# Kernel optimization log

Hardware: AMD Instinct MI355X
Metric: run time of the kernel (lower is better)

Reference implementation:

```python
import jax, jax.numpy as jnp
import numpy as np

B, T, D, H = 4, 2048, 1024, 16
HD = D // H  # head_dim = 64


def setup_inputs() -> dict:
    key = jax.random.key(0)
    ks = jax.random.split(key, 7)
    x = jax.random.normal(ks[0], (B, T, D), dtype=jnp.float32)
    engagement = jax.random.uniform(ks[1], (B, T), dtype=jnp.float32)
    mask = jax.random.uniform(ks[2], (B, T)) < 0.1  # True = masked-out key
    s = 1.0 / np.sqrt(D)
    qkv_w = jax.random.normal(ks[3], (3 * D, D), dtype=jnp.float32) * s
    qkv_b = jax.random.normal(ks[4], (3 * D,), dtype=jnp.float32) * 0.02
    out_w = jax.random.normal(ks[5], (D, D), dtype=jnp.float32) * s
    out_b = jax.random.normal(ks[6], (D,), dtype=jnp.float32) * 0.02
    return {"x": x, "engagement": engagement, "mask": mask,
            "qkv_w": qkv_w, "qkv_b": qkv_b, "out_w": out_w, "out_b": out_b}


def reference(x, engagement, mask, qkv_w, qkv_b, out_w, out_b):
    b, t, d = x.shape
    qkv = x @ qkv_w.T + qkv_b                       # [B,T,3D]
    q, k, v = jnp.split(qkv, 3, axis=-1)
    # [B,T,D] -> [B,H,T,HD]
    to_heads = lambda a: a.reshape(b, t, H, HD).transpose(0, 2, 1, 3)
    q, k, v = to_heads(q), to_heads(k), to_heads(v)
    attn = jnp.einsum('bhqd,bhkd->bhqk', q, k) / jnp.sqrt(jnp.float32(HD))
    log_g = jnp.log(jnp.clip(engagement, 1e-6))     # [B,T] per-key bias
    attn = attn + log_g[:, None, None, :]
    attn = jnp.where(mask[:, None, None, :], jnp.float32(-1e9), attn)
    p = jax.nn.softmax(attn, axis=-1)
    o = jnp.einsum('bhqk,bhkd->bhqd', p, v)         # [B,H,T,HD]
    o = o.transpose(0, 2, 1, 3).reshape(b, t, d)    # [B,T,D]
    return o @ out_w.T + out_b
```

## Files before the change

### kernel.cpp

```cpp
#include <hip/hip_runtime.h>
#include <math.h>

#define B_  4
#define T_  2048
#define D_  1024
#define H_  16
#define HD_ 64

typedef unsigned short ushort_t;
typedef unsigned int uint_t;
typedef __attribute__((ext_vector_type(8))) short bf16x8;
typedef __attribute__((ext_vector_type(4))) float f32x4;

#define SC_LOG2 0.1803368801111243f

__device__ inline ushort_t f2bf(float f) {
  uint_t u = __float_as_uint(f);
  u += 0x7fffu + ((u >> 16) & 1u);
  return (ushort_t)(u >> 16);
}
__device__ inline ushort_t f2bf_fast(float f) {
  return (ushort_t)((__float_as_uint(f) + 0x8000u) >> 16);
}
__device__ inline uint_t cvtpk_bf16(float lo, float hi) {
  uint_t r;
  asm("v_cvt_pk_bf16_f32 %0, %1, %2" : "=v"(r) : "v"(lo), "v"(hi));
  return r;
}

__device__ inline void gload_lds16(const ushort_t* g, ushort_t* l) {
  __builtin_amdgcn_global_load_lds(
      (const __attribute__((address_space(1))) unsigned int*)g,
      (__attribute__((address_space(3))) unsigned int*)l, 16, 0, 0);
}

__global__ __launch_bounds__(256) void cvt_bf16(const float* __restrict__ in,
                                                ushort_t* __restrict__ out, int n) {
  int i = (blockIdx.x * 256 + threadIdx.x) * 4;
  if (i + 3 < n) {
    float4 v = *(const float4*)(in + i);
    uint_t lo = (uint_t)f2bf(v.x) | ((uint_t)f2bf(v.y) << 16);
    uint_t hi = (uint_t)f2bf(v.z) | ((uint_t)f2bf(v.w) << 16);
    *(uint2*)(out + i) = make_uint2(lo, hi);
  }
}

__global__ __launch_bounds__(256) void bias_prep(const float* __restrict__ eng,
                                                 const int* __restrict__ mask,
                                                 float* __restrict__ biasA, int n) {
  int i = blockIdx.x * 256 + threadIdx.x;
  if (i < n) biasA[i] = mask[i] ? -1e30f : __log2f(fmaxf(eng[i], 1e-6f));
}

#define CHUNKS_ 32

#define STAGE_CHUNK(CK, SLOT)                                                  \
  {                                                                            \
    const int ck_ = (CK);                                                      \
    ushort_t* sb_ = lds + (SLOT) * SLOT_E;                                     \
    gload_lds16(Ag + (size_t)ck_ * 32, sb_ + w * 512);                         \
    if constexpr (BN == 256) {                                                 \
      gload_lds16(Bg + (size_t)ck_ * 32, sb_ + 4096 + w * 1024);               \
      gload_lds16(Bg + 16384 + (size_t)ck_ * 32, sb_ + 4096 + w * 1024 + 512); \
    } else {                                                                   \
      gload_lds16(Bg + (size_t)ck_ * 32, sb_ + 4096 + w * 512);                \
    }                                                                          \
  }

template <int WRITE_BF16, int BN>
__global__ __launch_bounds__(512, 4) void gemm256(
    const ushort_t* __restrict__ A, const ushort_t* __restrict__ Bm,
    const float* __restrict__ bias, void* __restrict__ Cout,
    int N, int nbx) {
  constexpr int SLOT_E = 4096 + BN * 32;
  constexpr int NBB = BN / 64;
  constexpr int WCOLS = BN / 4;
  __shared__ __align__(16) ushort_t lds[3 * SLOT_E];

  const int tid = threadIdx.x;
  const int w = tid >> 6, lane = tid & 63;
  const int l15 = lane & 15, quad = lane >> 4;
  const int wr = w >> 2, wc = w & 3;

  int wg = blockIdx.x;
  const int cpx = gridDim.x >> 3;
  wg = (wg & 7) * cpx + (wg >> 3);
  const int m0 = (wg / nbx) * 128, n0 = (wg % nbx) * BN;

  const int gc = (lane & 3) ^ ((lane >> 3) & 3);
  const ushort_t* Ag = A + (size_t)(m0 + w * 16 + (lane >> 2)) * 1024 + gc * 8;
  const ushort_t* Bg =
      Bm + (size_t)(n0 + w * (BN / 8) + (lane >> 2)) * 1024 + gc * 8;

  const int p8 = (quad ^ ((l15 >> 1) & 3)) * 8;
  const int rowA = (wr * 64 + l15) * 32 + p8;
  const int rowB = 4096 + (wc * WCOLS + l15) * 32 + p8;

  f32x4 acc[4][NBB];
#pragma unroll
  for (int mb = 0; mb < 4; ++mb)
#pragma unroll
    for (int nb = 0; nb < NBB; ++nb) acc[mb][nb] = (f32x4){0.f, 0.f, 0.f, 0.f};

  STAGE_CHUNK(0, 0);
  STAGE_CHUNK(1, 1);
  if constexpr (BN == 256)
    asm volatile("s_waitcnt vmcnt(3)" ::: "memory");
  else
    asm volatile("s_waitcnt vmcnt(2)" ::: "memory");
  __builtin_amdgcn_s_barrier();
  __builtin_amdgcn_sched_barrier(0);

  int s_cur = 0;
#pragma unroll 1
  for (int ph = 0; ph < CHUNKS_; ++ph) {
    const ushort_t* Ls = lds + s_cur * SLOT_E;
    bf16x8 af[4], bf[NBB];
#pragma unroll
    for (int mb = 0; mb < 4; ++mb)
      af[mb] = *(const bf16x8*)(Ls + rowA + mb * 512);
#pragma unroll
    for (int nb = 0; nb < NBB; ++nb)
      bf[nb] = *(const bf16x8*)(Ls + rowB + nb * 512);
    if (ph < CHUNKS_ - 2) {
      const int s_n2 = (s_cur == 0) ? 2 : s_cur - 1;
      STAGE_CHUNK(ph + 2, s_n2);
    }
    __builtin_amdgcn_s_setprio(1);
#pragma unroll
    for (int mb = 0; mb < 4; ++mb)
#pragma unroll
      for (int nb = 0; nb < NBB; ++nb)
        acc[mb][nb] = __builtin_amdgcn_mfma_f32_16x16x32_bf16(
            af[mb], bf[nb], acc[mb][nb], 0, 0, 0);
    __builtin_amdgcn_s_setprio(0);
    if (ph < CHUNKS_ - 2) {
      if constexpr (BN == 256)
        asm volatile("s_waitcnt vmcnt(3)" ::: "memory");
      else
        asm volatile("s_waitcnt vmcnt(2)" ::: "memory");
    } else {
      asm volatile("s_waitcnt vmcnt(0)" ::: "memory");
    }
    __builtin_amdgcn_s_barrier();
    __builtin_amdgcn_sched_barrier(0);
    s_cur = (s_cur == 2) ? 0 : s_cur + 1;
  }

  float bb[NBB];
#pragma unroll
  for (int nb = 0; nb < NBB; ++nb)
    bb[nb] = bias[n0 + wc * WCOLS + nb * 16 + l15];

  if constexpr (WRITE_BF16) {
    ushort_t* patch = lds + w * 4608;
    ushort_t* Cb = (ushort_t*)Cout;
#pragma unroll
    for (int mb = 0; mb < 4; ++mb)
#pragma unroll
      for (int nb = 0; nb < NBB; ++nb)
#pragma unroll
        for (int i = 0; i < 4; ++i)
          patch[(mb * 16 + quad * 4 + i) * 72 + nb * 16 + l15] =
              f2bf_fast(acc[mb][nb][i] + bb[nb]);
#pragma unroll
    for (int it = 0; it < 8; ++it) {
      int rl = it * 8 + (lane >> 3);
      size_t grow = (size_t)(m0 + wr * 64 + rl);
      uint4 v = *(const uint4*)&patch[rl * 72 + (lane & 7) * 8];
      *(uint4*)&Cb[grow * N + n0 + wc * WCOLS + (lane & 7) * 8] = v;
    }
  } else {
    float* Cf = (float*)Cout;
#pragma unroll
    for (int mb = 0; mb < 4; ++mb)
#pragma unroll
      for (int i = 0; i < 4; ++i) {
        size_t row = (size_t)(m0 + wr * 64 + mb * 16 + quad * 4 + i);
#pragma unroll
        for (int nb = 0; nb < NBB; ++nb)
          Cf[row * N + n0 + wc * WCOLS + nb * 16 + l15] =
              acc[mb][nb][i] + bb[nb];
      }
  }
}

#define ATTN_TILE(K0, Kc, Vc, bc, Kn, Vn, bn, PF)                              \
  {                                                                            \
    uint4 va_, vc_;                                                            \
    const bool pf_ = (PF);                                                     \
    if (pf_) {                                                                 \
      const int k1_ = (K0) + 64;                                               \
      gload_lds16(kbase + (size_t)(k1_ + w * 8 + kr8) * rs + kgc * 8,          \
                  &(Kn)[(w * 8) * 64]);                                        \
      if (tid < 256) {                                                         \
        const ushort_t* vp_ = vbase + (size_t)(k1_ + 2 * kp) * rs + cc * 8;    \
        va_ = *(const uint4*)vp_;                                              \
        vc_ = *(const uint4*)(vp_ + rs);                                       \
      }                                                                        \
      if (tid < 64) (bn)[tid] = bptr[k1_ + tid];                               \
    }                                                                          \
    bf16x8 kf0[4], kf1[4];                                                     \
    _Pragma("unroll")                                                          \
    for (int nb = 0; nb < 4; ++nb) {                                           \
      int key = nb * 16 + l15;                                                 \
      int p0 = (quad ^ (key & 7)) * 8;                                         \
      kf0[nb] = *(const bf16x8*)(&(Kc)[key * 64 + p0]);                        \
      kf1[nb] = *(const bf16x8*)(&(Kc)[key * 64 + (p0 ^ 32)]);                 \
    }                                                                          \
    bf16x8 vf0[4], vf1[4];                                                     \
    _Pragma("unroll")                                                          \
    for (int nbd = 0; nbd < 4; ++nbd) {                                        \
      vf0[nbd] = *(const bf16x8*)(&(Vc)[quad * 520 + (nbd * 16 + l15) * 8]);   \
      vf1[nbd] =                                                               \
          *(const bf16x8*)(&(Vc)[(4 + quad) * 520 + (nbd * 16 + l15) * 8]);    \
    }                                                                          \
    _Pragma("unroll")                                                          \
    for (int qb = 0; qb < 2; ++qb) {                                           \
      f32x4 st[4];                                                             \
      __builtin_amdgcn_s_setprio(1);                                           \
      _Pragma("unroll")                                                        \
      for (int nb = 0; nb < 4; ++nb) {                                         \
        f32x4 s = (f32x4){0.f, 0.f, 0.f, 0.f};                                 \
        s = __builtin_amdgcn_mfma_f32_16x16x32_bf16(kf0[nb], qf[qb][0], s, 0,  \
                                                    0, 0);                     \
        s = __builtin_amdgcn_mfma_f32_16x16x32_bf16(kf1[nb], qf[qb][1], s, 0,  \
                                                    0, 0);                     \
        st[nb] = s;                                                            \
      }                                                                        \
      __builtin_amdgcn_s_setprio(0);                                           \
      float pp[4][4];                                                          \
      float racc = 0.f;                                                        \
      _Pragma("unroll")                                                        \
      for (int nb = 0; nb < 4; ++nb) {                                         \
        f32x4 bv = *(const f32x4*)&(bc)[nb * 16 + quad * 4];                   \
        _Pragma("unroll")                                                      \
        for (int i = 0; i < 4; ++i) {                                          \
          float p = __builtin_amdgcn_exp2f(st[nb][i] * SC_LOG2 + bv[i]);       \
          pp[nb][i] = p;                                                       \
          racc += p;                                                           \
        }                                                                      \
      }                                                                        \
      rsum[qb] += racc;                                                        \
      union { uint4 u; bf16x8 v; } pf0, pf1;                                   \
      pf0.u.x = cvtpk_bf16(pp[0][0], pp[0][1]);                                \
      pf0.u.y = cvtpk_bf16(pp[0][2], pp[0][3]);                                \
      pf0.u.z = cvtpk_bf16(pp[1][0], pp[1][1]);                                \
      pf0.u.w = cvtpk_bf16(pp[1][2], pp[1][3]);                                \
      pf1.u.x = cvtpk_bf16(pp[2][0], pp[2][1]);                                \
      pf1.u.y = cvtpk_bf16(pp[2][2], pp[2][3]);                                \
      pf1.u.z = cvtpk_bf16(pp[3][0], pp[3][1]);                                \
      pf1.u.w = cvtpk_bf16(pp[3][2], pp[3][3]);                                \
      __builtin_amdgcn_s_setprio(1);                                           \
      _Pragma("unroll")                                                        \
      for (int nbd = 0; nbd < 4; ++nbd) {                                      \
        Oa[qb][nbd] = __builtin_amdgcn_mfma_f32_16x16x32_bf16(                 \
            pf0.v, vf0[nbd], Oa[qb][nbd], 0, 0, 0);                            \
        Oa[qb][nbd] = __builtin_amdgcn_mfma_f32_16x16x32_bf16(                 \
            pf1.v, vf1[nbd], Oa[qb][nbd], 0, 0, 0);                            \
      }                                                                        \
      __builtin_amdgcn_s_setprio(0);                                           \
    }                                                                          \
    if (pf_ && tid < 256) {                                                    \
      uint_t* dst_ = (uint_t*)&(Vn)[gp * 520 + cc * 64 + j0];                  \
      dst_[0]  = (va_.x & 0xffffu) | (vc_.x << 16);                            \
      dst_[4]  = (va_.x >> 16)     | (vc_.x & 0xffff0000u);                    \
      dst_[8]  = (va_.y & 0xffffu) | (vc_.y << 16);                            \
      dst_[12] = (va_.y >> 16)     | (vc_.y & 0xffff0000u);                    \
      dst_[16] = (va_.z & 0xffffu) | (vc_.z << 16);                            \
      dst_[20] = (va_.z >> 16)     | (vc_.z & 0xffff0000u);                    \
      dst_[24] = (va_.w & 0xffffu) | (vc_.w << 16);                            \
      dst_[28] = (va_.w >> 16)     | (vc_.w & 0xffff0000u);                    \
    }                                                                          \
    __syncthreads();                                                           \
  }

__global__ __launch_bounds__(512) void attn_mfma(
    const ushort_t* __restrict__ qkv, const float* __restrict__ biasA,
    ushort_t* __restrict__ oat) {
  __shared__ __align__(16) char smem[37888];
  ushort_t* Kb0 = (ushort_t*)(smem);
  ushort_t* Kb1 = (ushort_t*)(smem + 8192);
  ushort_t* Vb0 = (ushort_t*)(smem + 16384);
  ushort_t* Vb1 = (ushort_t*)(smem + 24704);
  float* bsh0 = (float*)(smem + 33024);
  float* bsh1 = (float*)(smem + 33280);
  float (*lsum)[32] = (float (*)[32])(smem + 36864);

  const int b = blockIdx.z, h = blockIdx.y;
  const int q0 = blockIdx.x * 256;
  const int tid = threadIdx.x;
  const int w = tid >> 6, lane = tid & 63;
  const int l15 = lane & 15, quad = lane >> 4;
  const size_t rs = 3 * D_;

  bf16x8 qf[2][2];
#pragma unroll
  for (int qb = 0; qb < 2; ++qb) {
    const ushort_t* qp =
        qkv + (size_t)(b * T_ + q0 + w * 32 + qb * 16 + l15) * rs + h * HD_;
    qf[qb][0] = *(const bf16x8*)(qp + quad * 8);
    qf[qb][1] = *(const bf16x8*)(qp + 32 + quad * 8);
  }

  f32x4 Oa[2][4];
#pragma unroll
  for (int qb = 0; qb < 2; ++qb)
#pragma unroll
    for (int nb = 0; nb < 4; ++nb) Oa[qb][nb] = (f32x4){0.f, 0.f, 0.f, 0.f};
  float rsum[2] = {0.f, 0.f};

  const ushort_t* kbase = qkv + (size_t)(b * T_) * rs + D_ + h * HD_;
  const ushort_t* vbase = kbase + D_;
  const float* bptr = biasA + b * T_;

  const int kr8 = lane >> 3;
  const int kgc = (lane & 7) ^ kr8;
  const int kp = tid & 31, cc = tid >> 5;
  const int gp = (kp >> 4) * 4 + ((kp >> 1) & 3);
  const int j0 = ((kp >> 3) & 1) * 4 + 2 * (kp & 1);

  {
    gload_lds16(kbase + (size_t)(w * 8 + kr8) * rs + kgc * 8,
                &Kb0[(w * 8) * 64]);
    if (tid < 256) {
      const ushort_t* vp = vbase + (size_t)(2 * kp) * rs + cc * 8;
      uint4 va = *(const uint4*)vp;
      uint4 vc = *(const uint4*)(vp + rs);
      uint_t* dst = (uint_t*)&Vb0[gp * 520 + cc * 64 + j0];
      dst[0]  = (va.x & 0xffffu) | (vc.x << 16);
      dst[4]  = (va.x >> 16)     | (vc.x & 0xffff0000u);
      dst[8]  = (va.y & 0xffffu) | (vc.y << 16);
      dst[12] = (va.y >> 16)     | (vc.y & 0xffff0000u);
      dst[16] = (va.z & 0xffffu) | (vc.z << 16);
      dst[20] = (va.z >> 16)     | (vc.z & 0xffff0000u);
      dst[24] = (va.w & 0xffffu) | (vc.w << 16);
      dst[28] = (va.w >> 16)     | (vc.w & 0xffff0000u);
    }
    if (tid < 64) bsh0[tid] = bptr[tid];
  }
  __syncthreads();

  for (int k0 = 0; k0 < T_; k0 += 128) {
    ATTN_TILE(k0,      Kb0, Vb0, bsh0, Kb1, Vb1, bsh1, true);
    ATTN_TILE(k0 + 64, Kb1, Vb1, bsh1, Kb0, Vb0, bsh0, k0 + 128 < T_);
  }

#pragma unroll
  for (int qb = 0; qb < 2; ++qb) {
    float r = rsum[qb];
    r += __shfl_xor(r, 16, 64);
    r += __shfl_xor(r, 32, 64);
    if (lane < 16) lsum[w][qb * 16 + lane] = r;
  }
  ushort_t* OstW = (ushort_t*)(smem) + w * 2304;
#pragma unroll
  for (int qb = 0; qb < 2; ++qb) {
    f32x4 lr = *(const f32x4*)&lsum[w][qb * 16 + quad * 4];
    f32x4 invl;
#pragma unroll
    for (int i = 0; i < 4; ++i) invl[i] = __builtin_amdgcn_rcpf(lr[i]);
#pragma unroll
    for (int nbd = 0; nbd < 4; ++nbd)
#pragma unroll
      for (int i = 0; i < 4; ++i)
        OstW[(qb * 16 + quad * 4 + i) * 72 + nbd * 16 + l15] =
            f2bf_fast(Oa[qb][nbd][i] * invl[i]);
  }
  ushort_t* dst = oat + (size_t)(b * T_ + q0 + w * 32) * D_ + h * HD_;
#pragma unroll
  for (int pp = 0; pp < 4; ++pp) {
    int row = pp * 8 + (lane >> 3), c = lane & 7;
    uint4 v = *(const uint4*)&OstW[row * 72 + c * 8];
    *(uint4*)&dst[(size_t)row * D_ + c * 8] = v;
  }
}

extern "C" void kernel_launch(void* const* d_in, const int* in_sizes, int n_in,
                              void* d_out, int out_size, void* d_ws, size_t ws_size,
                              hipStream_t stream) {
  const float* x     = (const float*)d_in[0];
  const float* eng   = (const float*)d_in[1];
  const int*   mask  = (const int*)d_in[2];
  const float* qkv_w = (const float*)d_in[3];
  const float* qkv_b = (const float*)d_in[4];
  const float* out_w = (const float*)d_in[5];
  const float* out_b = (const float*)d_in[6];
  float* out = (float*)d_out;

  const int M = B_ * T_;
  const size_t nx = (size_t)M * D_;
  const size_t nwq = (size_t)3 * D_ * D_;
  const size_t nwo = (size_t)D_ * D_;
  const size_t nqkv = (size_t)M * 3 * D_;

  char* p = (char*)d_ws;
  ushort_t* xb    = (ushort_t*)p;            p += nx * 2;
  ushort_t* wqkvb = (ushort_t*)p;            p += nwq * 2;
  ushort_t* woutb = (ushort_t*)p;            p += nwo * 2;
  ushort_t* qkvb  = (ushort_t*)p;            p += nqkv * 2;
  ushort_t* oatb  = (ushort_t*)p;            p += nx * 2;
  float*    biasA = (float*)p;               p += (size_t)M * 4;

  cvt_bf16<<<(int)(nx / 1024), 256, 0, stream>>>(x, xb, (int)nx);
  cvt_bf16<<<(int)(nwq / 1024), 256, 0, stream>>>(qkv_w, wqkvb, (int)nwq);
  cvt_bf16<<<(int)(nwo / 1024), 256, 0, stream>>>(out_w, woutb, (int)nwo);
  bias_prep<<<M / 256, 256, 0, stream>>>(eng, mask, biasA, M);

  gemm256<1, 256><<<768, 512, 0, stream>>>(xb, wqkvb, qkv_b, qkvb, 3 * D_, 12);
  attn_mfma<<<dim3(T_ / 256, H_, B_), 512, 0, stream>>>(qkvb, biasA, oatb);
  gemm256<0, 128><<<512, 512, 0, stream>>>(oatb, woutb, out_b, out, D_, 8);
}
```

Baseline: 282.6 us.

## Deepen GEMM LDS ring for narrow tiles and compute softmax row sums via MFMA

For the BN!=256 GEMM variant the LDS staging ring grows from 3 to 4 slots, prefetching three chunks ahead with matching vmcnt waits, to hide more global load latency. In attention, the per-row softmax denominator is accumulated with an extra MFMA against a ones vector instead of scalar adds plus a shuffle reduction through LDS. The attention kernel also gets a launch_bounds occupancy hint of 4. The ones-MFMA sums the bf16-rounded probabilities, which slightly changes numerics but matches what is multiplied into V. Costs are extra MFMA work and more LDS per GEMM block.

```diff
diff --git a/kernel.cpp b/kernel.cpp
--- a/kernel.cpp
+++ b/kernel.cpp
@@ -75,7 +75,9 @@
   constexpr int SLOT_E = 4096 + BN * 32;
   constexpr int NBB = BN / 64;
   constexpr int WCOLS = BN / 4;
-  __shared__ __align__(16) ushort_t lds[3 * SLOT_E];
+  constexpr int RING = (BN == 256) ? 3 : 4;
+  constexpr int LPC = (BN == 256) ? 3 : 2;
+  __shared__ __align__(16) ushort_t lds[RING * SLOT_E];
 
   const int tid = threadIdx.x;
   const int w = tid >> 6, lane = tid & 63;
@@ -104,10 +106,8 @@
 
   STAGE_CHUNK(0, 0);
   STAGE_CHUNK(1, 1);
-  if constexpr (BN == 256)
-    asm volatile("s_waitcnt vmcnt(3)" ::: "memory");
-  else
-    asm volatile("s_waitcnt vmcnt(2)" ::: "memory");
+  if constexpr (RING == 4) STAGE_CHUNK(2, 2);
+  asm volatile("s_waitcnt vmcnt(%0)" :: "i"((RING - 2) * LPC) : "memory");
   __builtin_amdgcn_s_barrier();
   __builtin_amdgcn_sched_barrier(0);
 
@@ -122,9 +122,10 @@
 #pragma unroll
     for (int nb = 0; nb < NBB; ++nb)
       bf[nb] = *(const bf16x8*)(Ls + rowB + nb * 512);
-    if (ph < CHUNKS_ - 2) {
-      const int s_n2 = (s_cur == 0) ? 2 : s_cur - 1;
-      STAGE_CHUNK(ph + 2, s_n2);
+    if (ph < CHUNKS_ - (RING - 1)) {
+      int s_st = s_cur + (RING - 1);
+      if (s_st >= RING) s_st -= RING;
+      STAGE_CHUNK(ph + (RING - 1), s_st);
     }
     __builtin_amdgcn_s_setprio(1);
 #pragma unroll
@@ -134,17 +135,21 @@
         acc[mb][nb] = __builtin_amdgcn_mfma_f32_16x16x32_bf16(
             af[mb], bf[nb], acc[mb][nb], 0, 0, 0);
     __builtin_amdgcn_s_setprio(0);
-    if (ph < CHUNKS_ - 2) {
-      if constexpr (BN == 256)
-        asm volatile("s_waitcnt vmcnt(3)" ::: "memory");
+    {
+      int rem = CHUNKS_ - 1 - ph;
+      int inflight = rem < (RING - 1) ? rem : (RING - 1);
+      int wait = (inflight - 1) * LPC;
+      if (wait < 0) wait = 0;
+      if (wait == (RING - 2) * LPC)
+        asm volatile("s_waitcnt vmcnt(%0)" :: "i"((RING - 2) * LPC) : "memory");
+      else if (RING == 4 && wait == LPC)
+        asm volatile("s_waitcnt vmcnt(%0)" :: "i"(LPC) : "memory");
       else
-        asm volatile("s_waitcnt vmcnt(2)" ::: "memory");
-    } else {
-      asm volatile("s_waitcnt vmcnt(0)" ::: "memory");
+        asm volatile("s_waitcnt vmcnt(0)" ::: "memory");
     }
     __builtin_amdgcn_s_barrier();
     __builtin_amdgcn_sched_barrier(0);
-    s_cur = (s_cur == 2) ? 0 : s_cur + 1;
+    s_cur = (s_cur == RING - 1) ? 0 : s_cur + 1;
   }
 
   float bb[NBB];
@@ -230,18 +235,13 @@
       }                                                                        \
       __builtin_amdgcn_s_setprio(0);                                           \
       float pp[4][4];                                                          \
-      float racc = 0.f;                                                        \
       _Pragma("unroll")                                                        \
       for (int nb = 0; nb < 4; ++nb) {                                         \
         f32x4 bv = *(const f32x4*)&(bc)[nb * 16 + quad * 4];                   \
         _Pragma("unroll")                                                      \
-        for (int i = 0; i < 4; ++i) {                                          \
-          float p = __builtin_amdgcn_exp2f(st[nb][i] * SC_LOG2 + bv[i]);       \
-          pp[nb][i] = p;                                                       \
-          racc += p;                                                           \
-        }                                                                      \
+        for (int i = 0; i < 4; ++i)                                            \
+          pp[nb][i] = __builtin_amdgcn_exp2f(st[nb][i] * SC_LOG2 + bv[i]);     \
       }                                                                        \
-      rsum[qb] += racc;                                                        \
       union { uint4 u; bf16x8 v; } pf0, pf1;                                   \
       pf0.u.x = cvtpk_bf16(pp[0][0], pp[0][1]);                                \
       pf0.u.y = cvtpk_bf16(pp[0][2], pp[0][3]);                                \
@@ -259,6 +259,10 @@
         Oa[qb][nbd] = __builtin_amdgcn_mfma_f32_16x16x32_bf16(                 \
             pf1.v, vf1[nbd], Oa[qb][nbd], 0, 0, 0);                            \
       }                                                                        \
+      Osum[qb] = __builtin_amdgcn_mfma_f32_16x16x32_bf16(                      \
+          pf0.v, onesf.v, Osum[qb], 0, 0, 0);                                  \
+      Osum[qb] = __builtin_amdgcn_mfma_f32_16x16x32_bf16(                      \
+          pf1.v, onesf.v, Osum[qb], 0, 0, 0);                                  \
       __builtin_amdgcn_s_setprio(0);                                           \
     }                                                                          \
     if (pf_ && tid < 256) {                                                    \
@@ -275,17 +279,16 @@
     __syncthreads();                                                           \
   }
 
-__global__ __launch_bounds__(512) void attn_mfma(
+__global__ __launch_bounds__(512, 4) void attn_mfma(
     const ushort_t* __restrict__ qkv, const float* __restrict__ biasA,
     ushort_t* __restrict__ oat) {
-  __shared__ __align__(16) char smem[37888];
+  __shared__ __align__(16) char smem[36864];
   ushort_t* Kb0 = (ushort_t*)(smem);
   ushort_t* Kb1 = (ushort_t*)(smem + 8192);
   ushort_t* Vb0 = (ushort_t*)(smem + 16384);
   ushort_t* Vb1 = (ushort_t*)(smem + 24704);
   float* bsh0 = (float*)(smem + 33024);
   float* bsh1 = (float*)(smem + 33280);
-  float (*lsum)[32] = (float (*)[32])(smem + 36864);
 
   const int b = blockIdx.z, h = blockIdx.y;
   const int q0 = blockIdx.x * 256;
@@ -303,12 +306,15 @@
     qf[qb][1] = *(const bf16x8*)(qp + 32 + quad * 8);
   }
 
-  f32x4 Oa[2][4];
-#pragma unroll
-  for (int qb = 0; qb < 2; ++qb)
+  f32x4 Oa[2][4], Osum[2];
+#pragma unroll
+  for (int qb = 0; qb < 2; ++qb) {
+    Osum[qb] = (f32x4){0.f, 0.f, 0.f, 0.f};
 #pragma unroll
     for (int nb = 0; nb < 4; ++nb) Oa[qb][nb] = (f32x4){0.f, 0.f, 0.f, 0.f};
-  float rsum[2] = {0.f, 0.f};
+  }
+  union { uint4 u; bf16x8 v; } onesf;
+  onesf.u = make_uint4(0x3F803F80u, 0x3F803F80u, 0x3F803F80u, 0x3F803F80u);
 
   const ushort_t* kbase = qkv + (size_t)(b * T_) * rs + D_ + h * HD_;
   const ushort_t* vbase = kbase + D_;
@@ -346,20 +352,12 @@
     ATTN_TILE(k0 + 64, Kb1, Vb1, bsh1, Kb0, Vb0, bsh0, k0 + 128 < T_);
   }
 
+  ushort_t* OstW = (ushort_t*)(smem) + w * 2304;
 #pragma unroll
   for (int qb = 0; qb < 2; ++qb) {
-    float r = rsum[qb];
-    r += __shfl_xor(r, 16, 64);
-    r += __shfl_xor(r, 32, 64);
-    if (lane < 16) lsum[w][qb * 16 + lane] = r;
-  }
-  ushort_t* OstW = (ushort_t*)(smem) + w * 2304;
-#pragma unroll
-  for (int qb = 0; qb < 2; ++qb) {
-    f32x4 lr = *(const f32x4*)&lsum[w][qb * 16 + quad * 4];
     f32x4 invl;
 #pragma unroll
-    for (int i = 0; i < 4; ++i) invl[i] = __builtin_amdgcn_rcpf(lr[i]);
+    for (int i = 0; i < 4; ++i) invl[i] = __builtin_amdgcn_rcpf(Osum[qb][i]);
 #pragma unroll
     for (int nbd = 0; nbd < 4; ++nbd)
 #pragma unroll
```

Result: slower. 545.5 us (+93.0%).
